# Optimization experiments

Hardware: AMD Instinct MI355X
Metric: run time of the kernel (lower is better)

## Reference

```python
import jax, jax.numpy as jnp
import numpy as np

NUM_HEADS = 32
NUM_KV_HEADS = 8
HEAD_DIM = 128
HIDDEN = 4096
BLOCK_SIZE = 16
NUM_BLOCKS = 512
BLOCKS_PER_REQ = 256
B, S = 1, 2048
ROPE_BASE = 10000.0


def _rope_cos_sin(seq_len, dim, dtype):
    inv_freq = 1.0 / (ROPE_BASE ** (jnp.arange(0, dim, 2, dtype=jnp.float32) / dim))
    t = jnp.arange(seq_len, dtype=jnp.float32)
    freqs = jnp.outer(t, inv_freq)            # [S, dim/2]
    emb = jnp.concatenate([freqs, freqs], -1)  # [S, dim]
    return jnp.cos(emb).astype(dtype), jnp.sin(emb).astype(dtype)


def _rotate_half(x):
    d = x.shape[-1] // 2
    return jnp.concatenate([-x[..., d:], x[..., :d]], axis=-1)


def setup_inputs() -> dict:
    key = jax.random.key(0)
    ks = jax.random.split(key, 6)
    sc = 0.02
    return {
        "hidden_states": jax.random.normal(ks[0], (B, S, HIDDEN), jnp.float32),
        "k_cache": jax.random.normal(ks[1], (NUM_BLOCKS, NUM_KV_HEADS, BLOCK_SIZE, HEAD_DIM), jnp.float32),
        "v_cache": jax.random.normal(ks[2], (NUM_BLOCKS, NUM_KV_HEADS, BLOCK_SIZE, HEAD_DIM), jnp.float32),
        "Wq": jax.random.normal(ks[3], (HIDDEN, HIDDEN), jnp.float32) * sc,
        "Wo": jax.random.normal(ks[4], (HIDDEN, HIDDEN), jnp.float32) * sc,
        "block_table": jax.random.randint(ks[5], (BLOCKS_PER_REQ,), 0, NUM_BLOCKS, jnp.int32),
    }


def reference(hidden_states, k_cache, v_cache, Wq, Wo, block_table):
    Bq, Sq, D = hidden_states.shape
    # query projection + reshape to [B, H, S, d]
    q = (hidden_states @ Wq.T).reshape(Bq, Sq, NUM_HEADS, HEAD_DIM).transpose(0, 2, 1, 3)
    cos, sin = _rope_cos_sin(Sq, HEAD_DIM, q.dtype)  # [S, d]
    q = q * cos[None, None] + _rotate_half(q) * sin[None, None]

    # paged KV gather: [n_blk, kvH, blk, d] -> [kvH, kv_len, d]
    kv_len = BLOCKS_PER_REQ * BLOCK_SIZE
    K = k_cache[block_table].transpose(1, 0, 2, 3).reshape(NUM_KV_HEADS, kv_len, HEAD_DIM)
    V = v_cache[block_table].transpose(1, 0, 2, 3).reshape(NUM_KV_HEADS, kv_len, HEAD_DIM)

    # GQA: repeat_interleave kv heads to q heads
    factor = NUM_HEADS // NUM_KV_HEADS
    K = jnp.repeat(K, factor, axis=0)[None]  # [1, H, kv_len, d]
    V = jnp.repeat(V, factor, axis=0)[None]

    scores = jnp.einsum('bhsd,bhkd->bhsk', q, K) / jnp.sqrt(jnp.asarray(HEAD_DIM, q.dtype))
    attn = jax.nn.softmax(scores, axis=-1)
    ctx = jnp.einsum('bhsk,bhkd->bhsd', attn, V)
    ctx = ctx.transpose(0, 2, 1, 3).reshape(Bq, Sq, D)
    return ctx @ Wo.T
```

## Files before the change

kernel.cpp:

```cpp
#include <hip/hip_runtime.h>
#include <hip/hip_bf16.h>

typedef __bf16 bf16;
typedef __bf16 bf16x4 __attribute__((ext_vector_type(4)));
typedef __bf16 bf16x8 __attribute__((ext_vector_type(8)));
typedef float f32x4 __attribute__((ext_vector_type(4)));

#define AS1 __attribute__((address_space(1)))
#define AS3 __attribute__((address_space(3)))
#define GLD16(gptr, lptr) \
  __builtin_amdgcn_global_load_lds((const AS1 unsigned int*)(gptr), \
                                   (AS3 unsigned int*)(lptr), 16, 0, 0)

#define NUM_H   32
#define NUM_KVH 8
#define DH      128
#define SEQ     2048
#define KVLEN   4096
#define HID     4096
#define RSCALE  0.08838834764831845f

__global__ void prep_hs(const float* __restrict__ hs, bf16* __restrict__ out) {
  int tid = blockIdx.x * 256 + threadIdx.x;
  size_t o = (size_t)tid * 8;
  float4 a = *(const float4*)(hs + o);
  float4 b = *(const float4*)(hs + o + 4);
  bf16x8 w = {(bf16)a.x, (bf16)a.y, (bf16)a.z, (bf16)a.w,
              (bf16)b.x, (bf16)b.y, (bf16)b.z, (bf16)b.w};
  *(bf16x8*)(out + o) = w;
}

__global__ void prep_k(const float* __restrict__ kc, const int* __restrict__ bt,
                       bf16* __restrict__ Kg) {
  int tid = blockIdx.x * 256 + threadIdx.x;
  int c   = tid & 31;
  int j   = (tid >> 5) & 4095;
  int kvh = tid >> 17;
  int blk = bt[j >> 4];
  float4 v = *(const float4*)(kc + (((size_t)blk * NUM_KVH + kvh) * 16 + (j & 15)) * DH + c * 4);
  bf16x4 w = {(bf16)v.x, (bf16)v.y, (bf16)v.z, (bf16)v.w};
  *(bf16x4*)(Kg + ((size_t)kvh * KVLEN + j) * DH + c * 4) = w;
}

__global__ void prep_v(const float* __restrict__ vc, const int* __restrict__ bt,
                       bf16* __restrict__ Vt) {
  __shared__ bf16 T[32][136];
  int e2 = blockIdx.x & 127, kvh = blockIdx.x >> 7;
  int t = threadIdx.x;
#pragma unroll
  for (int i = 0; i < 4; i++) {
    int idx = i * 256 + t;
    int pg  = idx >> 9;
    int pos = (idx >> 5) & 15;
    int c4  = idx & 31;
    int blk = bt[e2 * 2 + pg];
    float4 v = *(const float4*)(vc + (((size_t)blk * NUM_KVH + kvh) * 16 + pos) * DH + c4 * 4);
    bf16x4 w = {(bf16)v.x, (bf16)v.y, (bf16)v.z, (bf16)v.w};
    *(bf16x4*)(&T[pg * 16 + pos][c4 * 4]) = w;
  }
  __syncthreads();
  int d = t & 127, jc = t >> 7;
  bf16 tmp[16];
#pragma unroll
  for (int j = 0; j < 16; j++) tmp[j] = T[jc * 16 + j][d];
  bf16* dst = Vt + ((size_t)kvh * DH + d) * KVLEN + e2 * 32 + jc * 16;
  *(bf16x8*)dst = *(bf16x8*)tmp;
  *(bf16x8*)(dst + 8) = *(bf16x8*)(tmp + 8);
}

template <typename CT>
__global__ __launch_bounds__(256, 2)
void gemm_bb(const bf16* __restrict__ A, const bf16* __restrict__ B,
             CT* __restrict__ C, int M, int N, int K) {
  __shared__ alignas(16) bf16 As[2][128 * 64];
  __shared__ alignas(16) bf16 Bs[2][128 * 64];
  const int nwg = gridDim.x;
  const int q8  = nwg >> 3;
  const int wg  = ((int)blockIdx.x & 7) * q8 + ((int)blockIdx.x >> 3);
  const int nb = N >> 7;
  const int bm = wg / nb;
  const int bn = wg % nb;
  const int t = threadIdx.x;
  const int lane = t & 63, wave = t >> 6;
  const int lid = lane & 15, quad = lane >> 4;
  const int wm = (wave >> 1) * 64, wn = (wave & 1) * 64;
  const bf16* Ab = A + (size_t)bm * 128 * K;
  const bf16* Bb = B + (size_t)bn * 128 * K;
  f32x4 acc[4][4] = {};

  auto stage = [&](int buf, int k0) {
#pragma unroll
    for (int i = 0; i < 4; i++) {
      int id = i * 256 + t;
      int row = id >> 3, c = id & 7;
      int gc = c ^ (row & 7);
      GLD16(Ab + (size_t)row * K + k0 + gc * 8, &As[buf][id * 8]);
    }
#pragma unroll
    for (int i = 0; i < 4; i++) {
      int id = i * 256 + t;
      int row = id >> 3, c = id & 7;
      int gc = c ^ (row & 7);
      GLD16(Bb + (size_t)row * K + k0 + gc * 8, &Bs[buf][id * 8]);
    }
  };
  auto compute = [&](int buf) {
#pragma unroll
    for (int kk = 0; kk < 2; kk++) {
      bf16x8 af[4], bfr[4];
#pragma unroll
      for (int i = 0; i < 4; i++) {
        int row = wm + i * 16 + lid;
        af[i] = *(const bf16x8*)(&As[buf][row * 64 + ((kk * 4 + quad) ^ (row & 7)) * 8]);
      }
#pragma unroll
      for (int j = 0; j < 4; j++) {
        int row = wn + j * 16 + lid;
        bfr[j] = *(const bf16x8*)(&Bs[buf][row * 64 + ((kk * 4 + quad) ^ (row & 7)) * 8]);
      }
#pragma unroll
      for (int i = 0; i < 4; i++)
#pragma unroll
        for (int j = 0; j < 4; j++)
          acc[i][j] = __builtin_amdgcn_mfma_f32_16x16x32_bf16(bfr[j], af[i], acc[i][j], 0, 0, 0);
    }
  };

  stage(0, 0);
  __syncthreads();

  int cur = 0;
#pragma unroll 1
  for (int k0 = 64; k0 < K; k0 += 64) {
    stage(cur ^ 1, k0);
    __builtin_amdgcn_sched_barrier(0);
    compute(cur);
    __syncthreads();
    cur ^= 1;
  }
  compute(cur);

#pragma unroll
  for (int i = 0; i < 4; i++)
#pragma unroll
    for (int j = 0; j < 4; j++) {
      int m = bm * 128 + wm + i * 16 + lid;
      int n = bn * 128 + wn + j * 16 + quad * 4;
      if constexpr (sizeof(CT) == 4) {
        float4 w = {acc[i][j][0], acc[i][j][1], acc[i][j][2], acc[i][j][3]};
        *(float4*)(&C[(size_t)m * N + n]) = w;
      } else {
        bf16x4 w = {(bf16)acc[i][j][0], (bf16)acc[i][j][1],
                    (bf16)acc[i][j][2], (bf16)acc[i][j][3]};
        *(bf16x4*)(&C[(size_t)m * N + n]) = w;
      }
    }
}

__global__ void rope_q(bf16* __restrict__ Q) {
  __shared__ float tcs[64], tsn[64];
  int s = blockIdx.x;
  int t = threadIdx.x;
  if (t < 64) {
    float freq = expf(-(float)t * (logf(10000.f) / 64.f));
    float sn, cs;
    sincosf((float)s * freq, &sn, &cs);
    tsn[t] = sn; tcs[t] = cs;
  }
  __syncthreads();
  int h = t >> 3, d0 = (t & 7) * 8;
  bf16* ptr = Q + (size_t)s * HID + h * DH;
  bf16x8 lo = *(bf16x8*)(ptr + d0);
  bf16x8 hi = *(bf16x8*)(ptr + 64 + d0);
  bf16x8 olo, ohi;
#pragma unroll
  for (int e = 0; e < 8; e++) {
    float cs = tcs[d0 + e], sn = tsn[d0 + e];
    float q0 = (float)lo[e], q1 = (float)hi[e];
    olo[e] = (bf16)((q0 * cs - q1 * sn) * RSCALE);
    ohi[e] = (bf16)((q1 * cs + q0 * sn) * RSCALE);
  }
  *(bf16x8*)(ptr + d0) = olo;
  *(bf16x8*)(ptr + 64 + d0) = ohi;
}

__global__ __launch_bounds__(256, 2)
void attn(bf16* __restrict__ Q,
          const bf16* __restrict__ Kg,
          const bf16* __restrict__ Vt) {
  __shared__ alignas(16) bf16 Ks[2][64 * 128];
  __shared__ alignas(16) bf16 Vs[2][128 * 64];
  __shared__ alignas(16) bf16 Ps[4][2][1024];
  const int bid = ((int)blockIdx.x & 7) * 64 + ((int)blockIdx.x >> 3);
  const int h = bid >> 4, qt2 = bid & 15;
  const int kvh = h >> 2;
  const int t = threadIdx.x;
  const int wave = t >> 6, lane = t & 63;
  const int lid = lane & 15, quad = lane >> 4;

  bf16x8 qf[2][4];
#pragma unroll
  for (int x = 0; x < 2; x++) {
    const bf16* qb = Q + (size_t)(qt2 * 128 + x * 64 + wave * 16 + lid) * HID + h * DH;
#pragma unroll
    for (int kc = 0; kc < 4; kc++) qf[x][kc] = *(const bf16x8*)(qb + kc * 32 + quad * 8);
  }
  const bf16* Kh = Kg + (size_t)kvh * KVLEN * DH;
  const bf16* Vh = Vt + (size_t)kvh * DH * KVLEN;
  f32x4 acc_o[2][8] = {};
  f32x4 lsum[2] = {};
  const bf16 one = (bf16)1.0f;
  const bf16x8 ones = {one, one, one, one, one, one, one, one};

  auto stage = [&](int buf, int kv0) {
#pragma unroll
    for (int i = 0; i < 4; i++) {
      int id = i * 256 + t;
      int row = id >> 4, cs = id & 15;
      int gc = cs ^ (row & 7);
      GLD16(Kh + (size_t)(kv0 + row) * DH + gc * 8, &Ks[buf][id * 8]);
    }
#pragma unroll
    for (int i = 0; i < 4; i++) {
      int id = i * 256 + t;
      int d = id >> 3, cs = id & 7;
      int gc = cs ^ (d & 7);
      GLD16(Vh + (size_t)d * KVLEN + kv0 + gc * 8, &Vs[buf][id * 8]);
    }
  };

  stage(0, 0);
  __syncthreads();

  int cur = 0;
#pragma unroll 1
  for (int kv0 = 0; kv0 < KVLEN; kv0 += 64) {
    if (kv0 + 64 < KVLEN) stage(cur ^ 1, kv0 + 64);
    __builtin_amdgcn_sched_barrier(0);

    f32x4 sv[2][4];
#pragma unroll
    for (int n = 0; n < 4; n++) {
      f32x4 s0 = {}, s1 = {};
      int row = n * 16 + lid;
#pragma unroll
      for (int kc = 0; kc < 4; kc++) {
        int cs = (kc * 4 + quad) ^ (row & 7);
        bf16x8 kf = *(const bf16x8*)(&Ks[cur][row * DH + cs * 8]);
        s0 = __builtin_amdgcn_mfma_f32_16x16x32_bf16(kf, qf[0][kc], s0, 0, 0, 0);
        s1 = __builtin_amdgcn_mfma_f32_16x16x32_bf16(kf, qf[1][kc], s1, 0, 0, 0);
      }
      sv[0][n] = s0; sv[1][n] = s1;
    }

#pragma unroll
    for (int x = 0; x < 2; x++)
#pragma unroll
      for (int n = 0; n < 4; n++) {
        bf16x4 w = {(bf16)__expf(sv[x][n][0]), (bf16)__expf(sv[x][n][1]),
                    (bf16)__expf(sv[x][n][2]), (bf16)__expf(sv[x][n][3])};
        int c = (2 * n + (quad >> 1)) ^ (lid & 7);
        *(bf16x4*)(&Ps[wave][x][lid * 64 + c * 8 + (quad & 1) * 4]) = w;
      }

    bf16x8 pf[2][2];
#pragma unroll
    for (int x = 0; x < 2; x++)
#pragma unroll
      for (int kvc = 0; kvc < 2; kvc++) {
        int c = (kvc * 4 + quad) ^ (lid & 7);
        pf[x][kvc] = *(const bf16x8*)(&Ps[wave][x][lid * 64 + c * 8]);
      }

#pragma unroll
    for (int x = 0; x < 2; x++) {
      lsum[x] = __builtin_amdgcn_mfma_f32_16x16x32_bf16(ones, pf[x][0], lsum[x], 0, 0, 0);
      lsum[x] = __builtin_amdgcn_mfma_f32_16x16x32_bf16(ones, pf[x][1], lsum[x], 0, 0, 0);
    }

#pragma unroll
    for (int dt = 0; dt < 8; dt++) {
      int d = dt * 16 + lid;
#pragma unroll
      for (int kvc = 0; kvc < 2; kvc++) {
        int cs = (kvc * 4 + quad) ^ (d & 7);
        bf16x8 vf = *(const bf16x8*)(&Vs[cur][d * 64 + cs * 8]);
        acc_o[0][dt] = __builtin_amdgcn_mfma_f32_16x16x32_bf16(vf, pf[0][kvc], acc_o[0][dt], 0, 0, 0);
        acc_o[1][dt] = __builtin_amdgcn_mfma_f32_16x16x32_bf16(vf, pf[1][kvc], acc_o[1][dt], 0, 0, 0);
      }
    }

    __syncthreads();
    cur ^= 1;
  }

#pragma unroll
  for (int x = 0; x < 2; x++) {
    float rinv = 1.0f / lsum[x][0];
    int q = qt2 * 128 + x * 64 + wave * 16 + lid;
#pragma unroll
    for (int dt = 0; dt < 8; dt++) {
      bf16x4 w = {(bf16)(acc_o[x][dt][0] * rinv), (bf16)(acc_o[x][dt][1] * rinv),
                  (bf16)(acc_o[x][dt][2] * rinv), (bf16)(acc_o[x][dt][3] * rinv)};
      *(bf16x4*)(&Q[(size_t)q * HID + h * DH + dt * 16 + quad * 4]) = w;
    }
  }
}

template <typename CT>
__global__ __launch_bounds__(512, 2)
void gemm_bt2(const bf16* __restrict__ A, const float* __restrict__ B,
              CT* __restrict__ C, int M, int N, int K) {
  __shared__ alignas(16) bf16 As[2][128 * 64];
  __shared__ alignas(16) bf16 Bs[2][256 * 64];
  const int nb = N >> 8;
  const int bm = (int)blockIdx.x / nb;
  const int bn = (int)blockIdx.x % nb;
  const int t = threadIdx.x;
  const int lane = t & 63, wave = t >> 6;
  const int lid = lane & 15, quad = lane >> 4;
  const int wm = (wave >> 2) * 64, wn = (wave & 3) * 64;
  const bf16*  Ab = A + (size_t)bm * 128 * K;
  const float* Bb = B + (size_t)bn * 256 * K;
  f32x4 acc[4][4] = {};
  float4 breg[4][2];

  auto issueA = [&](int buf, int k0) {
#pragma unroll
    for (int i = 0; i < 2; i++) {
      int id = i * 512 + t;
      int row = id >> 3, c = id & 7;
      int gc = c ^ (row & 7);
      GLD16(Ab + (size_t)row * K + k0 + gc * 8, &As[buf][id * 8]);
    }
  };
  auto loadB = [&](int k0) {
#pragma unroll
    for (int i = 0; i < 4; i++) {
      int id = i * 512 + t;
      int row = id >> 3, c = id & 7;
      const float* src = Bb + (size_t)row * K + k0 + c * 8;
      breg[i][0] = *(const float4*)(src);
      breg[i][1] = *(const float4*)(src + 4);
    }
  };
  auto writeB = [&](int buf) {
#pragma unroll
    for (int i = 0; i < 4; i++) {
      int id = i * 512 + t;
      int row = id >> 3, c = id & 7;
      int sc = c ^ (row & 7);
      float4 u = breg[i][0], v = breg[i][1];
      bf16x8 w = {(bf16)u.x, (bf16)u.y, (bf16)u.z, (bf16)u.w,
                  (bf16)v.x, (bf16)v.y, (bf16)v.z, (bf16)v.w};
      *(bf16x8*)(&Bs[buf][row * 64 + sc * 8]) = w;
    }
  };
  auto compute = [&](int buf) {
#pragma unroll
    for (int kk = 0; kk < 2; kk++) {
      bf16x8 af[4], bfr[4];
#pragma unroll
      for (int i = 0; i < 4; i++) {
        int row = wm + i * 16 + lid;
        af[i] = *(const bf16x8*)(&As[buf][row * 64 + ((kk * 4 + quad) ^ (row & 7)) * 8]);
      }
#pragma unroll
      for (int j = 0; j < 4; j++) {
        int row = wn + j * 16 + lid;
        bfr[j] = *(const bf16x8*)(&Bs[buf][row * 64 + ((kk * 4 + quad) ^ (row & 7)) * 8]);
      }
#pragma unroll
      for (int i = 0; i < 4; i++)
#pragma unroll
        for (int j = 0; j < 4; j++)
          acc[i][j] = __builtin_amdgcn_mfma_f32_16x16x32_bf16(af[i], bfr[j], acc[i][j], 0, 0, 0);
    }
  };

  issueA(0, 0);
  loadB(0);
  writeB(0);
  __syncthreads();

  int cur = 0;
#pragma unroll 1
  for (int k0 = 64; k0 < K; k0 += 64) {
    issueA(cur ^ 1, k0);
    loadB(k0);
    __builtin_amdgcn_sched_barrier(0);
    compute(cur);
    __builtin_amdgcn_sched_barrier(0);
    writeB(cur ^ 1);
    __syncthreads();
    cur ^= 1;
  }
  compute(cur);

#pragma unroll
  for (int i = 0; i < 4; i++)
#pragma unroll
    for (int j = 0; j < 4; j++)
#pragma unroll
      for (int r = 0; r < 4; r++) {
        int m = bm * 128 + wm + i * 16 + quad * 4 + r;
        int n = bn * 256 + wn + j * 16 + lid;
        C[(size_t)m * N + n] = (CT)acc[i][j][r];
      }
}

extern "C" void kernel_launch(void* const* d_in, const int* in_sizes, int n_in,
                              void* d_out, int out_size, void* d_ws, size_t ws_size,
                              hipStream_t stream) {
  const float* hs  = (const float*)d_in[0];
  const float* kca = (const float*)d_in[1];
  const float* vca = (const float*)d_in[2];
  const float* Wq  = (const float*)d_in[3];
  const float* Wo  = (const float*)d_in[4];
  const int*   bt  = (const int*)d_in[5];
  float* out = (float*)d_out;

  bf16* Qlin  = (bf16*)d_ws;
  bf16* Kg    = (bf16*)d_out;
  bf16* Vt    = (bf16*)((char*)d_out + (8u << 20));
  bf16* hs_bf = (bf16*)((char*)d_out + (16u << 20));

  prep_k<<<4096, 256, 0, stream>>>(kca, bt, Kg);
  prep_v<<<1024, 256, 0, stream>>>(vca, bt, Vt);
  prep_hs<<<4096, 256, 0, stream>>>(hs, hs_bf);

  if (ws_size >= (80u << 20)) {
    bf16* Wq_bf = (bf16*)((char*)d_ws + (16u << 20));
    bf16* Wo_bf = (bf16*)((char*)d_ws + (48u << 20));
    prep_hs<<<8192, 256, 0, stream>>>(Wq, Wq_bf);
    prep_hs<<<8192, 256, 0, stream>>>(Wo, Wo_bf);
    gemm_bb<bf16><<<512, 256, 0, stream>>>(hs_bf, Wq_bf, Qlin, SEQ, HID, HID);
    rope_q<<<SEQ, 256, 0, stream>>>(Qlin);
    attn<<<512, 256, 0, stream>>>(Qlin, Kg, Vt);
    gemm_bb<float><<<512, 256, 0, stream>>>(Qlin, Wo_bf, out, SEQ, HID, HID);
  } else {
    gemm_bt2<bf16><<<256, 512, 0, stream>>>(hs_bf, Wq, Qlin, SEQ, HID, HID);
    rope_q<<<SEQ, 256, 0, stream>>>(Qlin);
    attn<<<512, 256, 0, stream>>>(Qlin, Kg, Vt);
    gemm_bt2<float><<<256, 512, 0, stream>>>(Qlin, Wo, out, SEQ, HID, HID);
  }
}
```

Before: 522.9 us.

## Use partial vmcnt waits with raw barriers for prefetch overlap; merge weight casts

Replaces __syncthreads in the GEMM and attention main loops with explicit s_waitcnt vmcnt(8) plus s_barrier. The loop now waits only for the current buffer's async global-to-LDS loads, leaving the next stage's loads in flight while computing. Also fuses the two weight-conversion launches into one kernel to save a launch. The hand-written waitcnt counts depend on the exact number of loads issued per stage (8) and could race if that changes.

```diff
diff --git a/kernel.cpp b/kernel.cpp
--- a/kernel.cpp
+++ b/kernel.cpp
@@ -28,6 +28,20 @@
   bf16x8 w = {(bf16)a.x, (bf16)a.y, (bf16)a.z, (bf16)a.w,
               (bf16)b.x, (bf16)b.y, (bf16)b.z, (bf16)b.w};
   *(bf16x8*)(out + o) = w;
+}
+
+__global__ void prep_w2(const float* __restrict__ Wq, const float* __restrict__ Wo,
+                        bf16* __restrict__ Qo, bf16* __restrict__ Oo) {
+  int half = blockIdx.x & 8191;
+  const float* src = (blockIdx.x < 8192) ? Wq : Wo;
+  bf16* dst = (blockIdx.x < 8192) ? Qo : Oo;
+  int tid = half * 256 + threadIdx.x;
+  size_t o = (size_t)tid * 8;
+  float4 a = *(const float4*)(src + o);
+  float4 b = *(const float4*)(src + o + 4);
+  bf16x8 w = {(bf16)a.x, (bf16)a.y, (bf16)a.z, (bf16)a.w,
+              (bf16)b.x, (bf16)b.y, (bf16)b.z, (bf16)b.w};
+  *(bf16x8*)(dst + o) = w;
 }
 
 __global__ void prep_k(const float* __restrict__ kc, const int* __restrict__ bt,
@@ -127,17 +141,22 @@
   };
 
   stage(0, 0);
-  __syncthreads();
-
   int cur = 0;
 #pragma unroll 1
   for (int k0 = 64; k0 < K; k0 += 64) {
     stage(cur ^ 1, k0);
+    asm volatile("s_waitcnt vmcnt(8)" ::: "memory");
+    __builtin_amdgcn_s_barrier();
     __builtin_amdgcn_sched_barrier(0);
     compute(cur);
-    __syncthreads();
+    __builtin_amdgcn_sched_barrier(0);
+    asm volatile("s_waitcnt lgkmcnt(0)" ::: "memory");
+    __builtin_amdgcn_s_barrier();
     cur ^= 1;
   }
+  asm volatile("s_waitcnt vmcnt(0)" ::: "memory");
+  __builtin_amdgcn_s_barrier();
+  __builtin_amdgcn_sched_barrier(0);
   compute(cur);
 
 #pragma unroll
@@ -230,12 +249,16 @@
   };
 
   stage(0, 0);
-  __syncthreads();
-
   int cur = 0;
 #pragma unroll 1
   for (int kv0 = 0; kv0 < KVLEN; kv0 += 64) {
-    if (kv0 + 64 < KVLEN) stage(cur ^ 1, kv0 + 64);
+    if (kv0 + 64 < KVLEN) {
+      stage(cur ^ 1, kv0 + 64);
+      asm volatile("s_waitcnt vmcnt(8)" ::: "memory");
+    } else {
+      asm volatile("s_waitcnt vmcnt(0)" ::: "memory");
+    }
+    __builtin_amdgcn_s_barrier();
     __builtin_amdgcn_sched_barrier(0);
 
     f32x4 sv[2][4];
@@ -290,7 +313,9 @@
       }
     }
 
-    __syncthreads();
+    __builtin_amdgcn_sched_barrier(0);
+    asm volatile("s_waitcnt lgkmcnt(0)" ::: "memory");
+    __builtin_amdgcn_s_barrier();
     cur ^= 1;
   }
 
@@ -432,8 +457,7 @@
   if (ws_size >= (80u << 20)) {
     bf16* Wq_bf = (bf16*)((char*)d_ws + (16u << 20));
     bf16* Wo_bf = (bf16*)((char*)d_ws + (48u << 20));
-    prep_hs<<<8192, 256, 0, stream>>>(Wq, Wq_bf);
-    prep_hs<<<8192, 256, 0, stream>>>(Wo, Wo_bf);
+    prep_w2<<<16384, 256, 0, stream>>>(Wq, Wo, Wq_bf, Wo_bf);
     gemm_bb<bf16><<<512, 256, 0, stream>>>(hs_bf, Wq_bf, Qlin, SEQ, HID, HID);
     rope_q<<<SEQ, 256, 0, stream>>>(Qlin);
     attn<<<512, 256, 0, stream>>>(Qlin, Kg, Vt);
```

Measured after the change: 520.3 us. Within noise of the previous version (-0.5%).
